# Kernel tuning notes

Measured on AMD Instinct MI355X. Metric: run time of the kernel, lower is better.

The kernel has to match this reference:

```python
import jax, jax.numpy as jnp
import numpy as np

N = 8192          # number of nodes
A = 3             # number of adjacency relations
D_IN = 256
D_OUT = 64


def setup_inputs() -> dict:
    key = jax.random.key(0)
    k1, k2, k3, k4 = jax.random.split(key, 4)
    inputs = jax.random.normal(k1, (N, D_IN), dtype=jnp.float32)
    # dense adjacency stack [A, N, N] (weighted graph)
    adj_set = jax.random.uniform(k2, (A, N, N), dtype=jnp.float32)
    att = jax.random.uniform(k3, (A,), dtype=jnp.float32)
    w = jax.random.normal(k4, (D_IN, D_OUT), dtype=jnp.float32) * (1.0 / np.sqrt(D_IN))
    b = jnp.zeros((D_OUT,), dtype=jnp.float32)
    return {"inputs": inputs, "adj_set": adj_set, "att": att, "w": w, "b": b}


def reference(inputs, adj_set, att, w, b):
    # dropout=False -> identity; note: self.relu is never applied in forward
    support = jnp.matmul(inputs, w) + b                      # [N, D_OUT]
    # outputs = sum_i att[i] * (adj_i @ support), fused as one einsum
    outputs = jnp.einsum("a,anm,md->nd", att, adj_set, support)
    return outputs
```

## Files before the change

### kernel.cpp

```cpp
#include <hip/hip_runtime.h>
#include <hip/hip_bf16.h>


#define NNODES 8192
#define DIN    256
#define DOUT   64
#define NA     3
#define KSTACK (NA * NNODES)
#define BK     512
#define NCHUNK (KSTACK / BK)
#define STRIP  16
#define LDSROW (BK + 8)

typedef float f32x4 __attribute__((ext_vector_type(4)));
typedef short s16x8 __attribute__((ext_vector_type(8)));
typedef short s16x4 __attribute__((ext_vector_type(4)));

__device__ __forceinline__ unsigned short f2bf(float f) {
    __hip_bfloat16 h = __float2bfloat16(f);
    return __builtin_bit_cast(unsigned short, h);
}

__device__ __forceinline__ s16x4 pack4(f32x4 v) {
    s16x4 w;
    w[0] = (short)f2bf(v[0]); w[1] = (short)f2bf(v[1]);
    w[2] = (short)f2bf(v[2]); w[3] = (short)f2bf(v[3]);
    return w;
}

__global__ __launch_bounds__(256) void prep_support(
    const float* __restrict__ x, const float* __restrict__ w,
    const float* __restrict__ bias, const float* __restrict__ att,
    unsigned short* __restrict__ Bp)
{
    const int t = threadIdx.x;
    const int d = t & 63;
    const int m = (blockIdx.x << 2) + (t >> 6);

    const float* xr = x + (size_t)m * DIN;
    float acc = bias[d];
#pragma unroll 4
    for (int k = 0; k < DIN; k += 4) {
        f32x4 xv = *(const f32x4*)(xr + k);
        acc += xv[0] * w[(k + 0) * DOUT + d];
        acc += xv[1] * w[(k + 1) * DOUT + d];
        acc += xv[2] * w[(k + 2) * DOUT + d];
        acc += xv[3] * w[(k + 3) * DOUT + d];
    }

    const int kt   = m >> 5;
    const int kl   = m & 31;
    const int lane = ((kl >> 3) << 4) | (d & 15);
    const int j    = kl & 7;
    const int nt   = d >> 4;

    const size_t base    = (size_t)(kt * 4 + nt) * 512 + lane * 8 + j;
    const size_t aStride = (size_t)(NNODES / 32) * 4 * 512;

    const float a0 = att[0], a1 = att[1], a2 = att[2];
    Bp[base]               = f2bf(a0 * acc);
    Bp[base + aStride]     = f2bf(a1 * acc);
    Bp[base + 2 * aStride] = f2bf(a2 * acc);
}

__global__ __launch_bounds__(256, 4) void graphconv_gemm(
    const float* __restrict__ adj, const unsigned short* __restrict__ Bp,
    float* __restrict__ out)
{
    __shared__ unsigned short lds[2][STRIP][LDSROW];

    const int tid  = threadIdx.x;
    const int wave = tid >> 6;
    const int lane = tid & 63;
    const int r    = lane & 15;
    const int g    = lane >> 4;
    const int strip = blockIdx.x;
    const int row0  = strip * STRIP;

    const s16x8* __restrict__ Bv = (const s16x8*)Bp;

    f32x4 acc0 = {0.f, 0.f, 0.f, 0.f};
    f32x4 acc1 = {0.f, 0.f, 0.f, 0.f};
    f32x4 acc2 = {0.f, 0.f, 0.f, 0.f};
    f32x4 acc3 = {0.f, 0.f, 0.f, 0.f};

    {
        const float* ab = adj;
#pragma unroll
        for (int p = 0; p < 4; ++p) {
            const int lr = wave * 4 + p;
            const float* rp = ab + (size_t)(row0 + lr) * NNODES + lane * 4;
            f32x4 v0 = __builtin_nontemporal_load((const f32x4*)rp);
            f32x4 v1 = __builtin_nontemporal_load((const f32x4*)(rp + 256));
            *(s16x4*)&lds[0][lr][lane * 4]       = pack4(v0);
            *(s16x4*)&lds[0][lr][256 + lane * 4] = pack4(v1);
        }
    }

#pragma unroll 2
    for (int c = 0; c < NCHUNK; ++c) {
        __syncthreads();
        const int cur = c & 1;

        f32x4 nv0[4], nv1[4];
        const bool more = (c + 1 < NCHUNK);
        if (more) {
            const int cn = c + 1;
            const float* ab = adj + ((size_t)(cn >> 4) << 26)
                                  + ((size_t)(cn & 15) << 9);
#pragma unroll
            for (int p = 0; p < 4; ++p) {
                const int lr = wave * 4 + p;
                const float* rp = ab + (size_t)(row0 + lr) * NNODES + lane * 4;
                nv0[p] = __builtin_nontemporal_load((const f32x4*)rp);
                nv1[p] = __builtin_nontemporal_load((const f32x4*)(rp + 256));
            }
        }

        const s16x8* bp = Bv + ((size_t)c * 16 + wave * 4) * 256 + lane;
#pragma unroll
        for (int t = 0; t < 4; ++t) {
            const s16x8 af = *(const s16x8*)&lds[cur][r][wave * 128 + t * 32 + g * 8];
            s16x8 b0 = bp[0];
            s16x8 b1 = bp[64];
            s16x8 b2 = bp[128];
            s16x8 b3 = bp[192];
            acc0 = __builtin_amdgcn_mfma_f32_16x16x32_bf16(af, b0, acc0, 0, 0, 0);
            acc1 = __builtin_amdgcn_mfma_f32_16x16x32_bf16(af, b1, acc1, 0, 0, 0);
            acc2 = __builtin_amdgcn_mfma_f32_16x16x32_bf16(af, b2, acc2, 0, 0, 0);
            acc3 = __builtin_amdgcn_mfma_f32_16x16x32_bf16(af, b3, acc3, 0, 0, 0);
            bp += 256;
        }

        if (more) {
#pragma unroll
            for (int p = 0; p < 4; ++p) {
                const int lr = wave * 4 + p;
                *(s16x4*)&lds[cur ^ 1][lr][lane * 4]       = pack4(nv0[p]);
                *(s16x4*)&lds[cur ^ 1][lr][256 + lane * 4] = pack4(nv1[p]);
            }
        }
    }

    __syncthreads();
    float* red = (float*)&lds[0][0][0];
#pragma unroll
    for (int j = 0; j < 4; ++j) {
        const int row = (g << 2) + j;
        float* rp = red + ((wave * 16 + row) << 6) + r;
        rp[0]  = acc0[j];
        rp[16] = acc1[j];
        rp[32] = acc2[j];
        rp[48] = acc3[j];
    }
    __syncthreads();

    const f32x4* redv = (const f32x4*)red;
    f32x4 s = redv[tid] + redv[256 + tid] + redv[512 + tid] + redv[768 + tid];
    ((f32x4*)out)[(strip << 8) + tid] = s;
}

extern "C" void kernel_launch(void* const* d_in, const int* in_sizes, int n_in,
                              void* d_out, int out_size, void* d_ws, size_t ws_size,
                              hipStream_t stream) {
    const float* x   = (const float*)d_in[0];
    const float* adj = (const float*)d_in[1];
    const float* att = (const float*)d_in[2];
    const float* w   = (const float*)d_in[3];
    const float* b   = (const float*)d_in[4];
    float* out = (float*)d_out;
    unsigned short* Bp = (unsigned short*)d_ws;

    prep_support<<<NNODES / 4, 256, 0, stream>>>(x, w, b, att, Bp);
    graphconv_gemm<<<NNODES / STRIP, 256, 0, stream>>>(adj, Bp, out);
}
```

Measured before the change: 219.6 us.

## Double K-chunk size and stagger chunk start per block to spread DRAM traffic

```diff
diff --git a/kernel.cpp b/kernel.cpp
--- a/kernel.cpp
+++ b/kernel.cpp
@@ -7,8 +7,9 @@
 #define DOUT   64
 #define NA     3
 #define KSTACK (NA * NNODES)
-#define BK     512
-#define NCHUNK (KSTACK / BK)
+#define BK     1024
+#define CPA    (NNODES / BK)
+#define NCHUNK (NA * CPA)
 #define STRIP  16
 #define LDSROW (BK + 8)
 
@@ -63,7 +64,7 @@
     Bp[base + 2 * aStride] = f2bf(a2 * acc);
 }
 
-__global__ __launch_bounds__(256, 4) void graphconv_gemm(
+__global__ __launch_bounds__(256, 2) void graphconv_gemm(
     const float* __restrict__ adj, const unsigned short* __restrict__ Bp,
     float* __restrict__ out)
 {
@@ -76,6 +77,7 @@
     const int g    = lane >> 4;
     const int strip = blockIdx.x;
     const int row0  = strip * STRIP;
+    const int c0    = blockIdx.x % NCHUNK;
 
     const s16x8* __restrict__ Bv = (const s16x8*)Bp;
 
@@ -85,42 +87,43 @@
     f32x4 acc3 = {0.f, 0.f, 0.f, 0.f};
 
     {
-        const float* ab = adj;
+        const float* ab = adj + ((size_t)(c0 >> 3) << 26) + ((size_t)(c0 & 7) << 10);
 #pragma unroll
         for (int p = 0; p < 4; ++p) {
-            const int lr = wave * 4 + p;
+            const int lr = (wave << 2) + p;
             const float* rp = ab + (size_t)(row0 + lr) * NNODES + lane * 4;
-            f32x4 v0 = __builtin_nontemporal_load((const f32x4*)rp);
-            f32x4 v1 = __builtin_nontemporal_load((const f32x4*)(rp + 256));
-            *(s16x4*)&lds[0][lr][lane * 4]       = pack4(v0);
-            *(s16x4*)&lds[0][lr][256 + lane * 4] = pack4(v1);
+#pragma unroll
+            for (int q = 0; q < 4; ++q) {
+                f32x4 v = __builtin_nontemporal_load((const f32x4*)(rp + q * 256));
+                *(s16x4*)&lds[0][lr][(q << 8) + (lane << 2)] = pack4(v);
+            }
         }
     }
 
-#pragma unroll 2
-    for (int c = 0; c < NCHUNK; ++c) {
+    int c = c0;
+    for (int i = 0; i < NCHUNK; ++i) {
+        const int cur = i & 1;
         __syncthreads();
-        const int cur = c & 1;
 
-        f32x4 nv0[4], nv1[4];
-        const bool more = (c + 1 < NCHUNK);
+        const int cn = (c == NCHUNK - 1) ? 0 : c + 1;
+        f32x4 nv[4][4];
+        const bool more = (i + 1 < NCHUNK);
         if (more) {
-            const int cn = c + 1;
-            const float* ab = adj + ((size_t)(cn >> 4) << 26)
-                                  + ((size_t)(cn & 15) << 9);
+            const float* ab = adj + ((size_t)(cn >> 3) << 26) + ((size_t)(cn & 7) << 10);
 #pragma unroll
             for (int p = 0; p < 4; ++p) {
-                const int lr = wave * 4 + p;
+                const int lr = (wave << 2) + p;
                 const float* rp = ab + (size_t)(row0 + lr) * NNODES + lane * 4;
-                nv0[p] = __builtin_nontemporal_load((const f32x4*)rp);
-                nv1[p] = __builtin_nontemporal_load((const f32x4*)(rp + 256));
+#pragma unroll
+                for (int q = 0; q < 4; ++q)
+                    nv[p][q] = __builtin_nontemporal_load((const f32x4*)(rp + q * 256));
             }
         }
 
-        const s16x8* bp = Bv + ((size_t)c * 16 + wave * 4) * 256 + lane;
-#pragma unroll
-        for (int t = 0; t < 4; ++t) {
-            const s16x8 af = *(const s16x8*)&lds[cur][r][wave * 128 + t * 32 + g * 8];
+        const s16x8* bp = Bv + ((size_t)(c << 5) + (wave << 3)) * 256 + lane;
+#pragma unroll 4
+        for (int t = 0; t < 8; ++t) {
+            const s16x8 af = *(const s16x8*)&lds[cur][r][(wave << 8) + (t << 5) + (g << 3)];
             s16x8 b0 = bp[0];
             s16x8 b1 = bp[64];
             s16x8 b2 = bp[128];
@@ -135,11 +138,14 @@
         if (more) {
 #pragma unroll
             for (int p = 0; p < 4; ++p) {
-                const int lr = wave * 4 + p;
-                *(s16x4*)&lds[cur ^ 1][lr][lane * 4]       = pack4(nv0[p]);
-                *(s16x4*)&lds[cur ^ 1][lr][256 + lane * 4] = pack4(nv1[p]);
+                const int lr = (wave << 2) + p;
+#pragma unroll
+                for (int q = 0; q < 4; ++q)
+                    *(s16x4*)&lds[cur ^ 1][lr][(q << 8) + (lane << 2)] = pack4(nv[p][q]);
             }
         }
+
+        c = cn;
     }
 
     __syncthreads();
```

New measurement: 226.8 us. 1.03x slower.
